# Performance work log

Hardware: AMD Instinct MI355X
Metric: run time of the kernel (lower is better)

The kernel has to match this reference:

```python
import jax, jax.numpy as jnp
import numpy as np

H, KV, D, HID, FF = 32, 8, 128, 4096, 14336
EPS = 1e-5
ROPE_THETA = 1e9


def setup_inputs() -> dict:
    key = jax.random.key(0)
    ks = jax.random.split(key, 10)
    B, S = 1, 2048
    s = 0.02
    return {
        "hidden_states": jax.random.normal(ks[0], (B, S, HID), dtype=jnp.float32),
        "wq": jax.random.normal(ks[1], (HID, H * D), dtype=jnp.float32) * s,
        "wk": jax.random.normal(ks[2], (HID, KV * D), dtype=jnp.float32) * s,
        "wv": jax.random.normal(ks[3], (HID, KV * D), dtype=jnp.float32) * s,
        "wo": jax.random.normal(ks[4], (H * D, HID), dtype=jnp.float32) * s,
        "w_gate": jax.random.normal(ks[5], (HID, FF), dtype=jnp.float32) * s,
        "w_up": jax.random.normal(ks[6], (HID, FF), dtype=jnp.float32) * s,
        "w_down": jax.random.normal(ks[7], (FF, HID), dtype=jnp.float32) * s,
        "ln1_w": jnp.ones((HID,), dtype=jnp.float32),
        "ln2_w": jnp.ones((HID,), dtype=jnp.float32),
        "position_ids": jnp.arange(B * S, dtype=jnp.int32).reshape(B, S),
    }


def _rmsnorm(x, w):
    var = jnp.mean(jnp.square(x), axis=-1, keepdims=True)
    return x * jax.lax.rsqrt(var + EPS) * w


def _rope_cos_sin(position_ids):
    inv_freq = 1.0 / (ROPE_THETA ** (jnp.arange(0, D, 2, dtype=jnp.float32) / D))  # [D/2]
    ang = position_ids.astype(jnp.float32)[..., None] * inv_freq  # [B,S,D/2]
    ang = jnp.concatenate([ang, ang], axis=-1)  # [B,S,D]
    return jnp.cos(ang), jnp.sin(ang)


def _rotate_half(x):
    x1, x2 = x[..., : D // 2], x[..., D // 2:]
    return jnp.concatenate([-x2, x1], axis=-1)


def _apply_rope(x, cos, sin):
    # x: [B,S,h,D]; cos/sin: [B,S,D]
    c, s = cos[:, :, None, :], sin[:, :, None, :]
    return x * c + _rotate_half(x) * s


def reference(hidden_states, wq, wk, wv, wo, w_gate, w_up, w_down, ln1_w, ln2_w, position_ids):
    B, S, _ = hidden_states.shape
    G = H // KV  # query groups per kv head

    # --- attention block ---
    residual = hidden_states
    x = _rmsnorm(hidden_states, ln1_w)
    q = (x @ wq).reshape(B, S, H, D)
    k = (x @ wk).reshape(B, S, KV, D)
    v = (x @ wv).reshape(B, S, KV, D)

    cos, sin = _rope_cos_sin(position_ids)
    q = _apply_rope(q, cos, sin)
    k = _apply_rope(k, cos, sin)

    # GQA: group query heads over kv heads, [B,S,KV,G,D]
    qg = q.reshape(B, S, KV, G, D)
    scores = jnp.einsum("bqhgd,bkhd->bhgqk", qg, k) / jnp.sqrt(jnp.float32(D))
    causal = position_ids[:, :, None] >= position_ids[:, None, :]  # [B,S,S]
    scores = jnp.where(causal[:, None, None, :, :], scores, jnp.float32(-1e9))
    probs = jax.nn.softmax(scores, axis=-1)
    attn = jnp.einsum("bhgqk,bkhd->bqhgd", probs, v).reshape(B, S, H * D)
    hidden_states = residual + attn @ wo

    # --- MLP block (SwiGLU) ---
    residual = hidden_states
    x = _rmsnorm(hidden_states, ln2_w)
    mlp = (jax.nn.silu(x @ w_gate) * (x @ w_up)) @ w_down
    return residual + mlp
```

## Files before the change

### kernel.cpp

```cpp
#include <hip/hip_runtime.h>

typedef short bf16x8 __attribute__((ext_vector_type(8)));
typedef float f32x4 __attribute__((ext_vector_type(4)));

#define DEV __device__ __forceinline__

constexpr int SEQ = 2048;
constexpr int HID = 4096;
constexpr int NH  = 32;
constexpr int NKV = 8;
constexpr int DH  = 128;
constexpr int FF  = 14336;
constexpr int QKVN = NH * DH + 2 * NKV * DH;

DEV unsigned short f2bf(float f) {
  union { float f; unsigned u; } x; x.f = f;
  unsigned r = x.u + 0x7fffu + ((x.u >> 16) & 1u);
  return (unsigned short)(r >> 16);
}
DEV float bf2f(unsigned short u) {
  union { unsigned u; float f; } x; x.u = ((unsigned)u) << 16; return x.f;
}
DEV void gload16(const void* g, void* l) {
  __builtin_amdgcn_global_load_lds(
      (const __attribute__((address_space(1))) unsigned*)g,
      (__attribute__((address_space(3))) unsigned*)l, 16, 0, 0);
}

__global__ __launch_bounds__(256) void rmsnorm_kernel(
    const float* __restrict__ x, const float* __restrict__ w,
    unsigned short* __restrict__ out) {
  const int row = blockIdx.x;
  const int tid = threadIdx.x;
  const float* xr = x + (size_t)row * HID;
  float4 v[4];
  float ss = 0.f;
#pragma unroll
  for (int i = 0; i < 4; ++i) {
    v[i] = *(const float4*)(xr + i * 1024 + tid * 4);
    ss += v[i].x * v[i].x + v[i].y * v[i].y + v[i].z * v[i].z + v[i].w * v[i].w;
  }
#pragma unroll
  for (int m = 1; m < 64; m <<= 1) ss += __shfl_xor(ss, m);
  __shared__ float red[4];
  if ((tid & 63) == 0) red[tid >> 6] = ss;
  __syncthreads();
  float tot = red[0] + red[1] + red[2] + red[3];
  float rms = rsqrtf(tot / (float)HID + 1e-5f);
  unsigned short* orow = out + (size_t)row * HID;
#pragma unroll
  for (int i = 0; i < 4; ++i) {
    int base = i * 1024 + tid * 4;
    ushort4 o;
    o.x = f2bf(v[i].x * rms * w[base + 0]);
    o.y = f2bf(v[i].y * rms * w[base + 1]);
    o.z = f2bf(v[i].z * rms * w[base + 2]);
    o.w = f2bf(v[i].w * rms * w[base + 3]);
    *(ushort4*)(orow + base) = o;
  }
}

__global__ __launch_bounds__(256) void wtrans_kernel(
    const float* __restrict__ W, unsigned short* __restrict__ WT, int K,
    int N) {
  __shared__ unsigned short t[64][72];
  const int k0 = blockIdx.x * 64, n0 = blockIdx.y * 64;
  const int tid = threadIdx.x;
  const int tk = tid >> 4;
  const int tn4 = (tid & 15) * 4;
#pragma unroll
  for (int p = 0; p < 4; ++p) {
    int k = tk + p * 16;
    float4 v = *(const float4*)(W + (size_t)(k0 + k) * N + n0 + tn4);
    t[tn4 + 0][k] = f2bf(v.x);
    t[tn4 + 1][k] = f2bf(v.y);
    t[tn4 + 2][k] = f2bf(v.z);
    t[tn4 + 3][k] = f2bf(v.w);
  }
  __syncthreads();
#pragma unroll
  for (int p = 0; p < 4; ++p) {
    int n = tk + p * 16;
    ushort4 o = *(const ushort4*)&t[n][tn4];
    *(ushort4*)(WT + (size_t)(n0 + n) * K + k0 + tn4) = o;
  }
}

__global__ __launch_bounds__(256) void rope_kernel(unsigned short* __restrict__ x,
                                                   int nheads, int ld) {
  const int gid = blockIdx.x * 256 + threadIdx.x;
  const int i = gid & 63;
  const int t = gid >> 6;
  const int s = t / nheads;
  const int hh = t - s * nheads;
  float ang = (float)s * exp2f((float)i * (-29.897352853986263f / 64.f));
  float sn, cs;
  sincosf(ang, &sn, &cs);
  size_t base = (size_t)s * ld + hh * DH + i;
  float x1 = bf2f(x[base]);
  float x2 = bf2f(x[base + 64]);
  x[base]      = f2bf(x1 * cs - x2 * sn);
  x[base + 64] = f2bf(x2 * cs + x1 * sn);
}

__global__ __launch_bounds__(256) void silu_mul_kernel(
    const unsigned short* __restrict__ g, const unsigned short* __restrict__ u,
    unsigned short* __restrict__ out) {
  const size_t idx = ((size_t)blockIdx.x * 256 + threadIdx.x) * 4;
  ushort4 gv = *(const ushort4*)(g + idx);
  ushort4 uv = *(const ushort4*)(u + idx);
  float gf[4] = {bf2f(gv.x), bf2f(gv.y), bf2f(gv.z), bf2f(gv.w)};
  float uf[4] = {bf2f(uv.x), bf2f(uv.y), bf2f(uv.z), bf2f(uv.w)};
  ushort4 o;
  unsigned short* op = (unsigned short*)&o;
#pragma unroll
  for (int j = 0; j < 4; ++j) {
    float sl = gf[j] / (1.f + __expf(-gf[j]));
    op[j] = f2bf(sl * uf[j]);
  }
  *(ushort4*)(out + idx) = o;
}

template <int WROWS, int EPI>
__global__ __launch_bounds__(512, 2) void gemm8p_kernel(
    const unsigned short* __restrict__ A, const unsigned short* __restrict__ BT,
    void* __restrict__ Cv, const float* __restrict__ res, int gridM, int N,
    int K) {
  constexpr int BM = 2 * WROWS;
  constexpr int MF = WROWS / 32;
  constexpr int H  = 2 + BM / 128;
  constexpr int ABYTES = BM * 128;
  constexpr int BUFBYTES = ABYTES + 32768;
  __shared__ __align__(128) char sm[2 * BUFBYTES];

  const int tid  = threadIdx.x;
  const int lane = tid & 63;
  const int wv   = tid >> 6;
  const int nwg = gridDim.x;
  const int b = blockIdx.x;
  const int logical = (b & 7) * (nwg >> 3) + (b >> 3);
  const int m0 = (logical % gridM) * BM;
  const int n0 = (logical / gridM) * 256;
  const int wm = (wv >> 2) * WROWS;
  const int wn = (wv & 3) * 64;
  const int nt = K >> 6;

  const int srow = tid >> 3;
  const int scolb = (tid & 7) * 16;
  const int sldsbase = wv * 1024;

  auto stage = [&](int h, int t) {
    const int buf = t & 1;
    const int kt = t * 64;
    char* ldsOp;
    const unsigned short* g;
    int grow0, rowBase;
    if (h < 2) {
      ldsOp = sm + buf * BUFBYTES + ABYTES; g = BT; grow0 = n0; rowBase = h * 128;
    } else {
      ldsOp = sm + buf * BUFBYTES;          g = A;  grow0 = m0; rowBase = (h - 2) * 128;
    }
#pragma unroll
    for (int r = 0; r < 2; ++r) {
      int row = rowBase + r * 64 + srow;
      const char* gp = (const char*)g + ((size_t)(grow0 + row) * K + kt) * 2 +
                       (scolb ^ ((row & 7) << 4));
      gload16(gp, ldsOp + rowBase * 128 + r * 8192 + sldsbase);
    }
  };

  const int kb0 = (lane >> 4) * 16;
  const int lrow = lane & 15;
  auto ldA = [&](const char* sA, int mh, int mf, int ks) {
    int row = wm + mh * (WROWS / 2) + mf * 16 + lrow;
    return *(const bf16x8*)(sA + ((row * 128 + kb0 + ks * 64) ^ ((row & 7) << 4)));
  };
  auto ldB = [&](const char* sB, int j, int ks) {
    int col = wn + (j >> 1) * 32 + (j & 1) * 16 + lrow;
    return *(const bf16x8*)(sB + ((col * 128 + kb0 + ks * 64) ^ ((col & 7) << 4)));
  };

  f32x4 acc[2 * MF][4] = {};

#pragma unroll
  for (int h = 0; h < H; ++h) stage(h, 0);
#pragma unroll
  for (int h = 0; h < H - 1; ++h) stage(h, 1);
  if (H == 4) asm volatile("s_waitcnt vmcnt(6)" ::: "memory");
  else        asm volatile("s_waitcnt vmcnt(4)" ::: "memory");
  __builtin_amdgcn_s_barrier();

  for (int t = 0; t < nt; ++t) {
    const char* sA = sm + (t & 1) * BUFBYTES;
    const char* sB = sA + ABYTES;
    bf16x8 a[MF][2], bb[4][2];

#pragma unroll
    for (int mf = 0; mf < MF; ++mf) {
      a[mf][0] = ldA(sA, 0, mf, 0);
      a[mf][1] = ldA(sA, 0, mf, 1);
    }
#pragma unroll
    for (int j = 0; j < 4; ++j) {
      bb[j][0] = ldB(sB, j, 0);
      bb[j][1] = ldB(sB, j, 1);
    }
    if (t + 1 < nt) stage(H - 1, t + 1);
    __builtin_amdgcn_sched_barrier(0);
    __builtin_amdgcn_s_barrier();
    __builtin_amdgcn_s_setprio(1);
#pragma unroll
    for (int mf = 0; mf < MF; ++mf)
#pragma unroll
      for (int nf = 0; nf < 2; ++nf)
#pragma unroll
        for (int ks = 0; ks < 2; ++ks)
          acc[mf][nf] = __builtin_amdgcn_mfma_f32_16x16x32_bf16(
              a[mf][ks], bb[nf][ks], acc[mf][nf], 0, 0, 0);
    __builtin_amdgcn_s_setprio(0);
    __builtin_amdgcn_sched_barrier(0);
    __builtin_amdgcn_s_barrier();

    if (t + 2 < nt) stage(0, t + 2);
    __builtin_amdgcn_sched_barrier(0);
    __builtin_amdgcn_s_barrier();
    __builtin_amdgcn_s_setprio(1);
#pragma unroll
    for (int mf = 0; mf < MF; ++mf)
#pragma unroll
      for (int nf = 0; nf < 2; ++nf)
#pragma unroll
        for (int ks = 0; ks < 2; ++ks)
          acc[mf][2 + nf] = __builtin_amdgcn_mfma_f32_16x16x32_bf16(
              a[mf][ks], bb[2 + nf][ks], acc[mf][2 + nf], 0, 0, 0);
    __builtin_amdgcn_s_setprio(0);
    __builtin_amdgcn_sched_barrier(0);
    __builtin_amdgcn_s_barrier();

#pragma unroll
    for (int mf = 0; mf < MF; ++mf) {
      a[mf][0] = ldA(sA, 1, mf, 0);
      a[mf][1] = ldA(sA, 1, mf, 1);
    }
    if (t + 2 < nt) stage(1, t + 2);
    __builtin_amdgcn_sched_barrier(0);
    __builtin_amdgcn_s_barrier();
    __builtin_amdgcn_s_setprio(1);
#pragma unroll
    for (int mf = 0; mf < MF; ++mf)
#pragma unroll
      for (int nf = 0; nf < 2; ++nf)
#pragma unroll
        for (int ks = 0; ks < 2; ++ks)
          acc[MF + mf][nf] = __builtin_amdgcn_mfma_f32_16x16x32_bf16(
              a[mf][ks], bb[nf][ks], acc[MF + mf][nf], 0, 0, 0);
    __builtin_amdgcn_s_setprio(0);
    __builtin_amdgcn_sched_barrier(0);
    __builtin_amdgcn_s_barrier();

    if (H == 4 && t + 2 < nt) stage(2, t + 2);
    if (t + 2 < nt) {
      if (H == 4) asm volatile("s_waitcnt vmcnt(6)" ::: "memory");
      else        asm volatile("s_waitcnt vmcnt(4)" ::: "memory");
    } else {
      asm volatile("s_waitcnt vmcnt(0)" ::: "memory");
    }
    __builtin_amdgcn_sched_barrier(0);
    __builtin_amdgcn_s_barrier();
    __builtin_amdgcn_s_setprio(1);
#pragma unroll
    for (int mf = 0; mf < MF; ++mf)
#pragma unroll
      for (int nf = 0; nf < 2; ++nf)
#pragma unroll
        for (int ks = 0; ks < 2; ++ks)
          acc[MF + mf][2 + nf] = __builtin_amdgcn_mfma_f32_16x16x32_bf16(
              a[mf][ks], bb[2 + nf][ks], acc[MF + mf][2 + nf], 0, 0, 0);
    __builtin_amdgcn_s_setprio(0);
    __builtin_amdgcn_sched_barrier(0);
    __builtin_amdgcn_s_barrier();
  }

  const int rb = (lane >> 4) * 4;
#pragma unroll
  for (int i = 0; i < 2 * MF; ++i) {
    const int mh = i / MF, mf = i % MF;
#pragma unroll
    for (int j = 0; j < 4; ++j) {
#pragma unroll
      for (int r = 0; r < 4; ++r) {
        size_t row = (size_t)(m0 + wm + mh * (WROWS / 2) + mf * 16 + rb + r);
        size_t col = (size_t)(n0 + wn + (j >> 1) * 32 + (j & 1) * 16 + lrow);
        float vv = acc[i][j][r];
        if (EPI == 0) {
          ((unsigned short*)Cv)[row * N + col] = f2bf(vv);
        } else {
          ((float*)Cv)[row * N + col] = vv + res[row * N + col];
        }
      }
    }
  }
}

__global__ __launch_bounds__(512, 1) void attn_kernel(
    const unsigned short* __restrict__ QKV, unsigned short* __restrict__ Ob) {
  __shared__ __align__(128) char sm[114688];
  char* sQ  = sm;
  char* sK0 = sm + 32768;
  char* sK1 = sm + 49152;
  char* sV0 = sm + 65536;
  char* sV1 = sm + 81920;
  char* sP  = sm + 98304;
  const int tid  = threadIdx.x;
  const int lane = tid & 63;
  const int wv   = tid >> 6;
  const int logical = blockIdx.x;
  const int xr = 15 - (logical >> 5);
  const int h = logical & 31;
  const int qb0 = xr * 128;
  const int hkv = h >> 2;
  const int rbase = (lane >> 4) * 4;
  const int cbase = lane & 15;
  const unsigned short* Qp = QKV + h * DH;
  const unsigned short* Kp = QKV + NH * DH + hkv * DH;
  const unsigned short* Vp = QKV + NH * DH + NKV * DH + hkv * DH;

#pragma unroll
  for (int i = 0; i < 4; ++i) {
    int offs = i * 8192 + tid * 16;
    int row = offs >> 8, col = offs & 255;
    const char* gp = (const char*)Qp + ((size_t)(qb0 + row) * QKVN) * 2 +
                     (col ^ ((row & 15) << 4));
    gload16(gp, sQ + i * 8192 + wv * 1024);
  }

  auto stageK = [&](int t) {
    char* dst = (t & 1) ? sK1 : sK0;
    const int kt0 = t * 64;
#pragma unroll
    for (int i = 0; i < 2; ++i) {
      int offs = i * 8192 + tid * 16;
      int row = offs >> 8, col = offs & 255;
      const char* gp = (const char*)Kp + ((size_t)(kt0 + row) * QKVN) * 2 +
                       (col ^ ((row & 15) << 4));
      gload16(gp, dst + i * 8192 + wv * 1024);
    }
  };

  const int d4  = (tid & 31) * 4;
  const int kv4 = (tid >> 5) * 4;
  const int rot = (tid >> 1) & 3;
  auto loadV = [&](int t, ushort4* vr) {
    const unsigned short* g0 = Vp + (size_t)(t * 64 + kv4) * QKVN + d4;
#pragma unroll
    for (int k = 0; k < 4; ++k) vr[k] = *(const ushort4*)(g0 + (size_t)k * QKVN);
  };
  auto writeV = [&](int t, const ushort4* vr) {
    char* dst = (t & 1) ? sV1 : sV0;
    const unsigned short* a0 = (const unsigned short*)&vr[0];
    const unsigned short* a1 = (const unsigned short*)&vr[1];
    const unsigned short* a2 = (const unsigned short*)&vr[2];
    const unsigned short* a3 = (const unsigned short*)&vr[3];
#pragma unroll
    for (int j = 0; j < 4; ++j) {
      int jj = (j + rot) & 3;
      int dd = d4 + jj;
      uint2 pk;
      pk.x = (unsigned)a0[jj] | ((unsigned)a1[jj] << 16);
      pk.y = (unsigned)a2[jj] | ((unsigned)a3[jj] << 16);
      *(uint2*)(dst + ((dd * 128 + kv4 * 2) ^ ((dd & 7) << 4))) = pk;
    }
  };

  ushort4 vr[4];
  stageK(0);
  loadV(0, vr);
  asm volatile("s_waitcnt vmcnt(0)" ::: "memory");
  writeV(0, vr);
  __syncthreads();

  const int qrow = wv * 16 + (lane & 15);
  bf16x8 aq[4];
#pragma unroll
  for (int kk = 0; kk < 4; ++kk) {
    int kb = (lane >> 4) * 16 + kk * 64;
    aq[kk] = *(const bf16x8*)(sQ + ((qrow * 256 + kb) ^ ((qrow & 15) << 4)));
  }

  f32x4 oacc[8] = {};
  float m_r[4] = {-1e30f, -1e30f, -1e30f, -1e30f};
  float l_r[4] = {0.f, 0.f, 0.f, 0.f};
  const int ntiles = 2 * (xr + 1);

  for (int t = 0; t < ntiles; ++t) {
    const int kt0 = t * 64;
    const char* cK = (t & 1) ? sK1 : sK0;
    const char* cV = (t & 1) ? sV1 : sV0;
    if (t + 1 < ntiles) {
      stageK(t + 1);
      loadV(t + 1, vr);
    }

    f32x4 sacc[4] = {};
#pragma unroll
    for (int kk = 0; kk < 4; ++kk) {
      int kb = (lane >> 4) * 16 + kk * 64;
#pragma unroll
      for (int ni = 0; ni < 4; ++ni) {
        int krow = ni * 16 + (lane & 15);
        bf16x8 bk =
            *(const bf16x8*)(cK + ((krow * 256 + kb) ^ ((krow & 15) << 4)));
        sacc[ni] = __builtin_amdgcn_mfma_f32_16x16x32_bf16(aq[kk], bk,
                                                           sacc[ni], 0, 0, 0);
      }
    }

    const float scale = 0.08838834764831845f;
#pragma unroll
    for (int r = 0; r < 4; ++r) {
      int qg = qb0 + wv * 16 + rbase + r;
      float mx = -1e30f;
#pragma unroll
      for (int ni = 0; ni < 4; ++ni) {
        int cg = kt0 + ni * 16 + cbase;
        float sv = sacc[ni][r] * scale;
        sv = (cg <= qg) ? sv : -1e30f;
        sacc[ni][r] = sv;
        mx = fmaxf(mx, sv);
      }
      mx = fmaxf(mx, __shfl_xor(mx, 1));
      mx = fmaxf(mx, __shfl_xor(mx, 2));
      mx = fmaxf(mx, __shfl_xor(mx, 4));
      mx = fmaxf(mx, __shfl_xor(mx, 8));
      float mnew = fmaxf(m_r[r], mx);
      float sf = __expf(m_r[r] - mnew);
      m_r[r] = mnew;
      float rsum = 0.f;
#pragma unroll
      for (int ni = 0; ni < 4; ++ni) {
        float pv = __expf(sacc[ni][r] - mnew);
        sacc[ni][r] = pv;
        rsum += pv;
      }
      rsum += __shfl_xor(rsum, 1);
      rsum += __shfl_xor(rsum, 2);
      rsum += __shfl_xor(rsum, 4);
      rsum += __shfl_xor(rsum, 8);
      l_r[r] = l_r[r] * sf + rsum;
#pragma unroll
      for (int nt2 = 0; nt2 < 8; ++nt2) oacc[nt2][r] *= sf;
    }

    char* pw = sP + wv * 2048;
#pragma unroll
    for (int ni = 0; ni < 4; ++ni)
#pragma unroll
      for (int r = 0; r < 4; ++r) {
        int row = rbase + r;
        int cb2 = (ni * 16 + cbase) * 2;
        *(unsigned short*)(pw + ((row * 128 + cb2) ^ ((row & 7) << 4))) =
            f2bf(sacc[ni][r]);
      }
    asm volatile("s_waitcnt lgkmcnt(0)" ::: "memory");

#pragma unroll
    for (int kk = 0; kk < 2; ++kk) {
      int kb = (lane >> 4) * 16 + kk * 64;
      int prow = lane & 15;
      bf16x8 ap =
          *(const bf16x8*)(pw + ((prow * 128 + kb) ^ ((prow & 7) << 4)));
#pragma unroll
      for (int nt2 = 0; nt2 < 8; ++nt2) {
        int vrow = nt2 * 16 + (lane & 15);
        bf16x8 bv =
            *(const bf16x8*)(cV + ((vrow * 128 + kb) ^ ((vrow & 7) << 4)));
        oacc[nt2] =
            __builtin_amdgcn_mfma_f32_16x16x32_bf16(ap, bv, oacc[nt2], 0, 0, 0);
      }
    }

    if (t + 1 < ntiles) {
      asm volatile("s_waitcnt vmcnt(0)" ::: "memory");
      writeV(t + 1, vr);
    }
    __syncthreads();
  }

#pragma unroll
  for (int nt2 = 0; nt2 < 8; ++nt2)
#pragma unroll
    for (int r = 0; r < 4; ++r) {
      size_t row = (size_t)(qb0 + wv * 16 + rbase + r);
      int col = nt2 * 16 + cbase;
      Ob[row * (NH * DH) + h * DH + col] = f2bf(oacc[nt2][r] / l_r[r]);
    }
}

extern "C" void kernel_launch(void* const* d_in, const int* in_sizes, int n_in,
                              void* d_out, int out_size, void* d_ws,
                              size_t ws_size, hipStream_t stream) {
  const float* hs  = (const float*)d_in[0];
  const float* wq  = (const float*)d_in[1];
  const float* wk  = (const float*)d_in[2];
  const float* wvp = (const float*)d_in[3];
  const float* wo  = (const float*)d_in[4];
  const float* wg  = (const float*)d_in[5];
  const float* wu  = (const float*)d_in[6];
  const float* wd  = (const float*)d_in[7];
  const float* ln1 = (const float*)d_in[8];
  const float* ln2 = (const float*)d_in[9];

  char* p = (char*)d_ws;
  size_t need = 0;
  auto alloc = [&](size_t bytes) {
    char* r = p + need;
    need += (bytes + 255) & ~(size_t)255;
    return r;
  };
  unsigned short* T1   = (unsigned short*)alloc((size_t)FF * HID * 2);
  unsigned short* xn   = (unsigned short*)alloc((size_t)SEQ * HID * 2);
  unsigned short* qkv  = (unsigned short*)alloc((size_t)SEQ * QKVN * 2);
  unsigned short* ab   = (unsigned short*)alloc((size_t)SEQ * NH * DH * 2);
  float*          h2   = (float*)alloc((size_t)SEQ * HID * 4);
  unsigned short* xn2  = (unsigned short*)alloc((size_t)SEQ * HID * 2);
  unsigned short* gbuf = (unsigned short*)alloc((size_t)SEQ * FF * 2);
  unsigned short* ubuf = (unsigned short*)alloc((size_t)SEQ * FF * 2);
  if (need > ws_size) return;

  rmsnorm_kernel<<<SEQ, 256, 0, stream>>>(hs, ln1, xn);
  wtrans_kernel<<<dim3(HID / 64, HID / 64), 256, 0, stream>>>(wq, T1, HID, HID);
  wtrans_kernel<<<dim3(HID / 64, (NKV * DH) / 64), 256, 0, stream>>>(
      wk, T1 + (size_t)(NH * DH) * HID, HID, NKV * DH);
  wtrans_kernel<<<dim3(HID / 64, (NKV * DH) / 64), 256, 0, stream>>>(
      wvp, T1 + (size_t)(NH * DH + NKV * DH) * HID, HID, NKV * DH);
  gemm8p_kernel<128, 0><<<(SEQ / 256) * (QKVN / 256), 512, 0, stream>>>(
      xn, T1, qkv, nullptr, SEQ / 256, QKVN, HID);
  rope_kernel<<<(SEQ * NH * 64) / 256, 256, 0, stream>>>(qkv, NH, QKVN);
  rope_kernel<<<(SEQ * NKV * 64) / 256, 256, 0, stream>>>(qkv + NH * DH, NKV,
                                                          QKVN);
  attn_kernel<<<512, 512, 0, stream>>>(qkv, ab);
  wtrans_kernel<<<dim3(HID / 64, HID / 64), 256, 0, stream>>>(wo, T1, HID, HID);
  gemm8p_kernel<64, 1><<<(SEQ / 128) * (HID / 256), 512, 0, stream>>>(
      ab, T1, h2, hs, SEQ / 128, HID, HID);
  rmsnorm_kernel<<<SEQ, 256, 0, stream>>>(h2, ln2, xn2);
  wtrans_kernel<<<dim3(HID / 64, FF / 64), 256, 0, stream>>>(wg, T1, HID, FF);
  gemm8p_kernel<128, 0><<<(SEQ / 256) * (FF / 256), 512, 0, stream>>>(
      xn2, T1, gbuf, nullptr, SEQ / 256, FF, HID);
  wtrans_kernel<<<dim3(HID / 64, FF / 64), 256, 0, stream>>>(wu, T1, HID, FF);
  gemm8p_kernel<128, 0><<<(SEQ / 256) * (FF / 256), 512, 0, stream>>>(
      xn2, T1, ubuf, nullptr, SEQ / 256, FF, HID);
  silu_mul_kernel<<<((size_t)SEQ * FF) / 1024, 256, 0, stream>>>(gbuf, ubuf,
                                                                 gbuf);
  wtrans_kernel<<<dim3(FF / 64, HID / 64), 256, 0, stream>>>(wd, T1, FF, HID);
  gemm8p_kernel<64, 1><<<(SEQ / 128) * (HID / 256), 512, 0, stream>>>(
      gbuf, T1, d_out, h2, SEQ / 128, HID, FF);
}
```

Baseline: 1.301 ms.

## Split-K the O-proj and down-proj GEMMs with larger tiles and a combine kernel

The output-projection and down-projection GEMMs switch from 128x256 tiles over the full K to 256x256 tiles with K split in two, keeping the same block count. Each split writes fp32 partials into reused workspace buffers, and a new combine kernel adds the two partials and the residual. The aim is more operand reuse per block from the larger tile. The cost is extra global traffic to write and reread the fp32 partials, plus one more launch per GEMM. The second down-proj partial is written through a buffer that is smaller than the partial, so it runs into adjacent dead workspace.

```diff
diff --git a/kernel.cpp b/kernel.cpp
--- a/kernel.cpp
+++ b/kernel.cpp
@@ -121,11 +121,26 @@
   *(ushort4*)(out + idx) = o;
 }
 
+__global__ __launch_bounds__(256) void combine_kernel(
+    const float* __restrict__ p0, const float* __restrict__ p1,
+    const float* __restrict__ res, float* __restrict__ out) {
+  const size_t i = ((size_t)blockIdx.x * 256 + threadIdx.x) * 4;
+  float4 a = *(const float4*)(p0 + i);
+  float4 b = *(const float4*)(p1 + i);
+  float4 c = *(const float4*)(res + i);
+  float4 o;
+  o.x = a.x + b.x + c.x;
+  o.y = a.y + b.y + c.y;
+  o.z = a.z + b.z + c.z;
+  o.w = a.w + b.w + c.w;
+  *(float4*)(out + i) = o;
+}
+
 template <int WROWS, int EPI>
 __global__ __launch_bounds__(512, 2) void gemm8p_kernel(
     const unsigned short* __restrict__ A, const unsigned short* __restrict__ BT,
-    void* __restrict__ Cv, const float* __restrict__ res, int gridM, int N,
-    int K) {
+    void* __restrict__ Cv0, void* __restrict__ Cv1, int gridM, int N, int Kld,
+    int nsplit) {
   constexpr int BM = 2 * WROWS;
   constexpr int MF = WROWS / 32;
   constexpr int H  = 2 + BM / 128;
@@ -139,11 +154,16 @@
   const int nwg = gridDim.x;
   const int b = blockIdx.x;
   const int logical = (b & 7) * (nwg >> 3) + (b >> 3);
-  const int m0 = (logical % gridM) * BM;
-  const int n0 = (logical / gridM) * 256;
+  const int ntiles = nwg / nsplit;
+  const int s = logical / ntiles;
+  const int r = logical - s * ntiles;
+  const int m0 = (r % gridM) * BM;
+  const int n0 = (r / gridM) * 256;
+  const int Klen = Kld / nsplit;
+  const int koff = s * Klen;
   const int wm = (wv >> 2) * WROWS;
   const int wn = (wv & 3) * 64;
-  const int nt = K >> 6;
+  const int nt = Klen >> 6;
 
   const int srow = tid >> 3;
   const int scolb = (tid & 7) * 16;
@@ -151,7 +171,7 @@
 
   auto stage = [&](int h, int t) {
     const int buf = t & 1;
-    const int kt = t * 64;
+    const int kt = koff + t * 64;
     char* ldsOp;
     const unsigned short* g;
     int grow0, rowBase;
@@ -161,11 +181,11 @@
       ldsOp = sm + buf * BUFBYTES;          g = A;  grow0 = m0; rowBase = (h - 2) * 128;
     }
 #pragma unroll
-    for (int r = 0; r < 2; ++r) {
-      int row = rowBase + r * 64 + srow;
-      const char* gp = (const char*)g + ((size_t)(grow0 + row) * K + kt) * 2 +
+    for (int rr = 0; rr < 2; ++rr) {
+      int row = rowBase + rr * 64 + srow;
+      const char* gp = (const char*)g + ((size_t)(grow0 + row) * Kld + kt) * 2 +
                        (scolb ^ ((row & 7) << 4));
-      gload16(gp, ldsOp + rowBase * 128 + r * 8192 + sldsbase);
+      gload16(gp, ldsOp + rowBase * 128 + rr * 8192 + sldsbase);
     }
   };
 
@@ -282,20 +302,21 @@
   }
 
   const int rb = (lane >> 4) * 4;
+  float* P = (float*)(s ? Cv1 : Cv0);
 #pragma unroll
   for (int i = 0; i < 2 * MF; ++i) {
     const int mh = i / MF, mf = i % MF;
 #pragma unroll
     for (int j = 0; j < 4; ++j) {
 #pragma unroll
-      for (int r = 0; r < 4; ++r) {
-        size_t row = (size_t)(m0 + wm + mh * (WROWS / 2) + mf * 16 + rb + r);
+      for (int rr = 0; rr < 4; ++rr) {
+        size_t row = (size_t)(m0 + wm + mh * (WROWS / 2) + mf * 16 + rb + rr);
         size_t col = (size_t)(n0 + wn + (j >> 1) * 32 + (j & 1) * 16 + lrow);
-        float vv = acc[i][j][r];
+        float vv = acc[i][j][rr];
         if (EPI == 0) {
-          ((unsigned short*)Cv)[row * N + col] = f2bf(vv);
+          ((unsigned short*)Cv0)[row * N + col] = f2bf(vv);
         } else {
-          ((float*)Cv)[row * N + col] = vv + res[row * N + col];
+          P[row * N + col] = vv;
         }
       }
     }
@@ -527,6 +548,11 @@
   unsigned short* ubuf = (unsigned short*)alloc((size_t)SEQ * FF * 2);
   if (need > ws_size) return;
 
+  float* pO0 = (float*)gbuf;
+  float* pO1 = (float*)ubuf;
+  float* pD0 = (float*)ubuf;
+  float* pD1 = (float*)xn;
+
   rmsnorm_kernel<<<SEQ, 256, 0, stream>>>(hs, ln1, xn);
   wtrans_kernel<<<dim3(HID / 64, HID / 64), 256, 0, stream>>>(wq, T1, HID, HID);
   wtrans_kernel<<<dim3(HID / 64, (NKV * DH) / 64), 256, 0, stream>>>(
@@ -534,24 +560,27 @@
   wtrans_kernel<<<dim3(HID / 64, (NKV * DH) / 64), 256, 0, stream>>>(
       wvp, T1 + (size_t)(NH * DH + NKV * DH) * HID, HID, NKV * DH);
   gemm8p_kernel<128, 0><<<(SEQ / 256) * (QKVN / 256), 512, 0, stream>>>(
-      xn, T1, qkv, nullptr, SEQ / 256, QKVN, HID);
+      xn, T1, qkv, nullptr, SEQ / 256, QKVN, HID, 1);
   rope_kernel<<<(SEQ * NH * 64) / 256, 256, 0, stream>>>(qkv, NH, QKVN);
   rope_kernel<<<(SEQ * NKV * 64) / 256, 256, 0, stream>>>(qkv + NH * DH, NKV,
                                                           QKVN);
   attn_kernel<<<512, 512, 0, stream>>>(qkv, ab);
   wtrans_kernel<<<dim3(HID / 64, HID / 64), 256, 0, stream>>>(wo, T1, HID, HID);
-  gemm8p_kernel<64, 1><<<(SEQ / 128) * (HID / 256), 512, 0, stream>>>(
-      ab, T1, h2, hs, SEQ / 128, HID, HID);
+  gemm8p_kernel<128, 2><<<(SEQ / 256) * (HID / 256) * 2, 512, 0, stream>>>(
+      ab, T1, pO0, pO1, SEQ / 256, HID, HID, 2);
+  combine_kernel<<<(SEQ * HID) / 1024, 256, 0, stream>>>(pO0, pO1, hs, h2);
   rmsnorm_kernel<<<SEQ, 256, 0, stream>>>(h2, ln2, xn2);
   wtrans_kernel<<<dim3(HID / 64, FF / 64), 256, 0, stream>>>(wg, T1, HID, FF);
   gemm8p_kernel<128, 0><<<(SEQ / 256) * (FF / 256), 512, 0, stream>>>(
-      xn2, T1, gbuf, nullptr, SEQ / 256, FF, HID);
+      xn2, T1, gbuf, nullptr, SEQ / 256, FF, HID, 1);
   wtrans_kernel<<<dim3(HID / 64, FF / 64), 256, 0, stream>>>(wu, T1, HID, FF);
   gemm8p_kernel<128, 0><<<(SEQ / 256) * (FF / 256), 512, 0, stream>>>(
-      xn2, T1, ubuf, nullptr, SEQ / 256, FF, HID);
+      xn2, T1, ubuf, nullptr, SEQ / 256, FF, HID, 1);
   silu_mul_kernel<<<((size_t)SEQ * FF) / 1024, 256, 0, stream>>>(gbuf, ubuf,
                                                                  gbuf);
   wtrans_kernel<<<dim3(FF / 64, HID / 64), 256, 0, stream>>>(wd, T1, FF, HID);
-  gemm8p_kernel<64, 1><<<(SEQ / 128) * (HID / 256), 512, 0, stream>>>(
-      gbuf, T1, d_out, h2, SEQ / 128, HID, FF);
-}
+  gemm8p_kernel<128, 2><<<(SEQ / 256) * (HID / 256) * 2, 512, 0, stream>>>(
+      gbuf, T1, pD0, pD1, SEQ / 256, HID, FF, 2);
+  combine_kernel<<<(SEQ * HID) / 1024, 256, 0, stream>>>(pD0, pD1, h2,
+                                                         (float*)d_out);
+}
```

After: 1.305 ms. No clear change (+0.3%).
